# Kernel optimization log

Measured on AMD Instinct MI355X. Metric: run time of the kernel, lower is better.

## Reference

```python
import jax, jax.numpy as jnp
import numpy as np
from jax import lax

N_IN = 512      # n_input == n_output of decoder
N_H = 2048      # n_hidden
N_L = 2         # n_layers (encoder/decoder GRU stacks written out explicitly)
SEQ = 2048      # sequence length
SPARSITY = 0.1  # sparsity_level -> k_sparse = int(N_H * SPARSITY)


def setup_inputs() -> dict:
    key = jax.random.key(0)
    ks = jax.random.split(key, 14)
    s = 0.02
    f32 = jnp.float32
    return {
        "sequence": jax.random.normal(ks[0], (SEQ, N_IN), f32),
        # encoder GRU (pytorch layout: W_ih [3H, in], W_hh [3H, H], gate order r,z,n)
        "enc_Wih0": jax.random.normal(ks[1], (3 * N_H, N_IN), f32) * s,
        "enc_Wih1": jax.random.normal(ks[2], (3 * N_H, N_H), f32) * s,
        "enc_Whh": jax.random.normal(ks[3], (N_L, 3 * N_H, N_H), f32) * s,
        "enc_bih": jax.random.normal(ks[4], (N_L, 3 * N_H), f32) * s,
        "enc_bhh": jax.random.normal(ks[5], (N_L, 3 * N_H), f32) * s,
        # decoder GRU (input dim = N_IN)
        "dec_Wih0": jax.random.normal(ks[6], (3 * N_H, N_IN), f32) * s,
        "dec_Wih1": jax.random.normal(ks[7], (3 * N_H, N_H), f32) * s,
        "dec_Whh": jax.random.normal(ks[8], (N_L, 3 * N_H, N_H), f32) * s,
        "dec_bih": jax.random.normal(ks[9], (N_L, 3 * N_H), f32) * s,
        "dec_bhh": jax.random.normal(ks[10], (N_L, 3 * N_H), f32) * s,
        # decoder output Linear: n_hidden -> n_output
        "dec_Wout": jax.random.normal(ks[11], (N_IN, N_H), f32) * s,
        "dec_bout": jax.random.normal(ks[12], (N_IN,), f32) * s,
    }


def _gru_cell(x, h, Wih, Whh, bih, bhh):
    # x: [in], h: [H]; PyTorch GRU equations, gate order (r, z, n)
    gi = Wih @ x + bih
    gh = Whh @ h + bhh
    ir, iz, inn = jnp.split(gi, 3)
    hr, hz, hn = jnp.split(gh, 3)
    r = jax.nn.sigmoid(ir + hr)
    z = jax.nn.sigmoid(iz + hz)
    n = jnp.tanh(inn + r * hn)
    return (1.0 - z) * n + z * h


def reference(sequence, enc_Wih0, enc_Wih1, enc_Whh, enc_bih, enc_bhh,
              dec_Wih0, dec_Wih1, dec_Whh, dec_bih, dec_bhh,
              dec_Wout, dec_bout):
    seq_len = sequence.shape[0]

    # ---- encoder: 2-layer GRU over the sequence, batch=1 (batch dim dropped) ----
    def enc_step(h, x):
        h0 = _gru_cell(x, h[0], enc_Wih0, enc_Whh[0], enc_bih[0], enc_bhh[0])
        h1 = _gru_cell(h0, h[1], enc_Wih1, enc_Whh[1], enc_bih[1], enc_bhh[1])
        return jnp.stack([h0, h1]), None

    h0_init = jnp.zeros((N_L, N_H), sequence.dtype)
    enc_hidden, _ = lax.scan(enc_step, h0_init, sequence)

    # ---- top-k sparsity on innermost (last) layer of the hidden state ----
    k_sparse = int(N_H * SPARSITY)
    h_last = enc_hidden[N_L - 1]
    _, top_idx = lax.top_k(h_last, k_sparse)
    mask = jnp.zeros((N_H,), h_last.dtype).at[top_idx].set(1.0)
    enc_hidden = enc_hidden.at[N_L - 1].set(h_last * mask)

    # ---- decoder: seq_len-1 single-step GRU+Linear, targets are sequence reversed ----
    targets = jnp.flip(sequence[: seq_len - 1], axis=0)  # sequence[seq_len-2-i]

    def dec_step(carry, target):
        x, h = carry
        h0 = _gru_cell(x, h[0], dec_Wih0, dec_Whh[0], dec_bih[0], dec_bhh[0])
        h1 = _gru_cell(h0, h[1], dec_Wih1, dec_Whh[1], dec_bih[1], dec_bhh[1])
        out = dec_Wout @ h1 + dec_bout
        step_loss = jnp.mean((out - target) ** 2)
        return (out, jnp.stack([h0, h1])), (out, step_loss)

    init = (sequence[seq_len - 1], enc_hidden)
    _, (reconstructed, step_losses) = lax.scan(dec_step, init, targets)
    loss = jnp.sum(step_losses) / seq_len
    return reconstructed, loss
```

## Files before the change

kernel.cpp:

```cpp
#include <hip/hip_runtime.h>
#include <hip/hip_fp16.h>
#include <hip/hip_cooperative_groups.h>

namespace cg = cooperative_groups;

#define H      2048
#define NIN    512
#define TH     (3 * H)
#define SEQLEN 2048
#define KSP    204
#define NBLK   256
#define NTHR   512

typedef unsigned int uint32;

constexpr long O_EA = 0;
constexpr long O_EB = O_EA + 1572864;
constexpr long O_EC = O_EB + 6291456;
constexpr long O_ED = O_EC + 6291456;
constexpr long O_DA = O_ED + 6291456;
constexpr long O_DB = O_DA + 1572864;
constexpr long O_DC = O_DB + 6291456;
constexpr long O_DD = O_DC + 6291456;
constexpr long O_WO = O_DD + 6291456;
constexpr long U_TOTAL = O_WO + 524288;
constexpr size_t WS_STATE_BYTES = 65536;

struct Params {
    const float* seq;
    const float* eWih0; const float* eWih1; const float* eWhh;
    const float* ebih;  const float* ebhh;
    const float* dWih0; const float* dWih1; const float* dWhh;
    const float* dbih;  const float* dbhh;
    const float* dWout; const float* dbout;
    float* out;
    float* ws;
};

__device__ __forceinline__ float wave_reduce_f(float v) {
#pragma unroll
    for (int m = 32; m >= 1; m >>= 1) v += __shfl_xor(v, m, 64);
    return v;
}

__device__ __forceinline__ float sigmoidf_(float v) { return 1.f / (1.f + expf(-v)); }

__device__ __forceinline__ float2 h2f(uint32 u) {
    __half2 h = *reinterpret_cast<__half2*>(&u);
    return __half22float2(h);
}

__global__ void pack_kernel(const float* __restrict__ src, uint32* __restrict__ dst,
                            int total, int xdim, int nrows)
{
    int KK = xdim / 256;
    for (int i = blockIdx.x * blockDim.x + threadIdx.x; i < total;
         i += gridDim.x * blockDim.x) {
        int l = i & 63;
        int rest = i >> 6;
        int p2 = rest & 1; rest >>= 1;
        int kk = rest % KK; rest /= KK;
        int r  = rest % nrows; rest /= nrows;
        int j  = rest;
        int c0 = 256 * kk + 4 * l + 2 * p2;
        const float* row = src + ((size_t)r * H + j) * xdim;
        unsigned short b0 = __half_as_ushort(__float2half_rn(row[c0]));
        unsigned short b1 = __half_as_ushort(__float2half_rn(row[c0 + 1]));
        dst[i] = ((uint32)b1 << 16) | b0;
    }
}

template <int NU>
__device__ __forceinline__ void load_seg3(uint32 (&dst)[3][NU], const uint32* seg,
                                          int j, int lane)
{
#pragma unroll
    for (int r = 0; r < 3; ++r)
#pragma unroll
        for (int u = 0; u < NU; ++u)
            dst[r][u] = seg[((size_t)(j * 3 + r) * NU + u) * 64 + lane];
}

__device__ __forceinline__ void load_seg1(uint32 (&dst)[16], const uint32* seg,
                                          int j, int lane)
{
#pragma unroll
    for (int u = 0; u < 16; ++u)
        dst[u] = seg[((size_t)j * 16 + u) * 64 + lane];
}

template <int NU>
__device__ __forceinline__ void dot3h(const uint32 (&w)[3][NU],
                                      const float* __restrict__ vec, int lane,
                                      float acc[3])
{
#pragma unroll
    for (int kk = 0; kk < NU / 2; ++kk) {
        float4 v = ((const float4*)vec)[kk * 64 + lane];
#pragma unroll
        for (int r = 0; r < 3; ++r) {
            float2 lo = h2f(w[r][2 * kk]);
            float2 hi = h2f(w[r][2 * kk + 1]);
            acc[r] = fmaf(lo.x, v.x, acc[r]);
            acc[r] = fmaf(lo.y, v.y, acc[r]);
            acc[r] = fmaf(hi.x, v.z, acc[r]);
            acc[r] = fmaf(hi.y, v.w, acc[r]);
        }
    }
}

template <int NUX>
__device__ __forceinline__ float gru_cell_reg(int j, int lane,
    const uint32 (&wi)[3][NUX], const uint32 (&wh)[3][16],
    const float* __restrict__ x, const float* __restrict__ h,
    float bir, float biz, float bin, float bhr, float bhz, float bhn)
{
    float ai[3] = {0.f, 0.f, 0.f}, ah[3] = {0.f, 0.f, 0.f};
    dot3h<NUX>(wi, x, lane, ai);
    dot3h<16>(wh, h, lane, ah);
    float hj  = h[j];
    float sr  = wave_reduce_f(ai[0] + ah[0]);
    float sz  = wave_reduce_f(ai[1] + ah[1]);
    float sn  = wave_reduce_f(ai[2]);
    float shn = wave_reduce_f(ah[2]);
    float r = sigmoidf_(sr + bir + bhr);
    float z = sigmoidf_(sz + biz + bhz);
    float n = tanhf(sn + bin + r * (shn + bhn));
    return (1.f - z) * n + z * hj;
}

__global__ void __launch_bounds__(NTHR, 2)
seqae_reg_kernel(Params p)
{
    cg::grid_group grid = cg::this_grid();
    const int lane = threadIdx.x & 63;
    const int j    = blockIdx.x * (NTHR / 64) + (threadIdx.x >> 6);

    float* loss = p.ws;
    float* h0b[2] = { p.ws + 64, p.ws + 64 + H };
    float* h1b[2] = { p.ws + 64 + 2 * H, p.ws + 64 + 3 * H };
    const uint32* U = (const uint32*)((const char*)p.ws + WS_STATE_BYTES);

    {
        int gtid = blockIdx.x * NTHR + threadIdx.x;
        if (gtid == 0) *loss = 0.f;
        for (int i = gtid; i < H; i += NBLK * NTHR) { h0b[0][i] = 0.f; h1b[0][i] = 0.f; }
    }
    grid.sync();

    uint32 wa[3][4], wb[3][16], wc[3][16], wd[3][16];
    load_seg3<4>(wa, U + O_EA, j, lane);
    load_seg3<16>(wb, U + O_EB, j, lane);
    load_seg3<16>(wc, U + O_EC, j, lane);
    load_seg3<16>(wd, U + O_ED, j, lane);

    float eb[12];
    {
        const float* bi0 = p.ebih;      const float* bi1 = p.ebih + TH;
        const float* bh0 = p.ebhh;      const float* bh1 = p.ebhh + TH;
        eb[0] = bi0[j]; eb[1] = bi0[H + j]; eb[2] = bi0[2 * H + j];
        eb[3] = bh0[j]; eb[4] = bh0[H + j]; eb[5] = bh0[2 * H + j];
        eb[6] = bi1[j]; eb[7] = bi1[H + j]; eb[8] = bi1[2 * H + j];
        eb[9] = bh1[j]; eb[10] = bh1[H + j]; eb[11] = bh1[2 * H + j];
    }

    int c0 = 0, c1 = 0;

    for (int ph = 0; ph <= SEQLEN; ++ph) {
        const float* h0old = h0b[c0];
        float h0v = 0.f, h1v = 0.f;
        if (ph < SEQLEN)
            h0v = gru_cell_reg<4>(j, lane, wa, wb, p.seq + (size_t)ph * NIN, h0old,
                                  eb[0], eb[1], eb[2], eb[3], eb[4], eb[5]);
        if (ph >= 1)
            h1v = gru_cell_reg<16>(j, lane, wc, wd, h0old, h1b[c1],
                                   eb[6], eb[7], eb[8], eb[9], eb[10], eb[11]);
        if (lane == 0) {
            if (ph < SEQLEN) h0b[c0 ^ 1][j] = h0v;
            if (ph >= 1)     h1b[c1 ^ 1][j] = h1v;
        }
        grid.sync();
        if (ph < SEQLEN) c0 ^= 1;
        if (ph >= 1)     c1 ^= 1;
    }

    {
        const float* hs = h1b[c1];
        float vj = hs[j];
        int cnt = 0;
        for (int i = lane; i < H; i += 64) {
            float vi = hs[i];
            cnt += (vi > vj) || (vi == vj && i < j);
        }
#pragma unroll
        for (int m = 32; m >= 1; m >>= 1) cnt += __shfl_xor(cnt, m, 64);
        if (lane == 0) h1b[c1 ^ 1][j] = (cnt < KSP) ? vj : 0.f;
    }
    grid.sync();
    c1 ^= 1;

    load_seg3<4>(wa, U + O_DA, j, lane);
    load_seg3<16>(wb, U + O_DB, j, lane);
    load_seg3<16>(wc, U + O_DC, j, lane);
    load_seg3<16>(wd, U + O_DD, j, lane);
    uint32 wo[16];
    load_seg1(wo, U + O_WO, j & (NIN - 1), lane);

    float db[12], boutj;
    {
        const float* bi0 = p.dbih;      const float* bi1 = p.dbih + TH;
        const float* bh0 = p.dbhh;      const float* bh1 = p.dbhh + TH;
        db[0] = bi0[j]; db[1] = bi0[H + j]; db[2] = bi0[2 * H + j];
        db[3] = bh0[j]; db[4] = bh0[H + j]; db[5] = bh0[2 * H + j];
        db[6] = bi1[j]; db[7] = bi1[H + j]; db[8] = bi1[2 * H + j];
        db[9] = bh1[j]; db[10] = bh1[H + j]; db[11] = bh1[2 * H + j];
        boutj = p.dbout[j & (NIN - 1)];
    }

    float lsum = 0.f;
    for (int t = 0; t < SEQLEN - 1; ++t) {
        const float* x = (t == 0) ? (p.seq + (size_t)(SEQLEN - 1) * NIN)
                                  : (p.out + (size_t)(t - 1) * NIN);
        float h0v = gru_cell_reg<4>(j, lane, wa, wb, x, h0b[c0],
                                    db[0], db[1], db[2], db[3], db[4], db[5]);
        if (lane == 0) h0b[c0 ^ 1][j] = h0v;
        grid.sync(); c0 ^= 1;

        float h1v = gru_cell_reg<16>(j, lane, wc, wd, h0b[c0], h1b[c1],
                                     db[6], db[7], db[8], db[9], db[10], db[11]);
        if (lane == 0) h1b[c1 ^ 1][j] = h1v;
        grid.sync(); c1 ^= 1;

        if (j < NIN) {
            const float* h1n = h1b[c1];
            float a = 0.f;
#pragma unroll
            for (int kk = 0; kk < 8; ++kk) {
                float4 v = ((const float4*)h1n)[kk * 64 + lane];
                float2 lo = h2f(wo[2 * kk]);
                float2 hi = h2f(wo[2 * kk + 1]);
                a = fmaf(lo.x, v.x, a); a = fmaf(lo.y, v.y, a);
                a = fmaf(hi.x, v.z, a); a = fmaf(hi.y, v.w, a);
            }
            a = wave_reduce_f(a);
            float o = a + boutj;
            if (lane == 0) p.out[(size_t)t * NIN + j] = o;
            float tg = p.seq[(size_t)(SEQLEN - 2 - t) * NIN + j];
            float d = o - tg;
            lsum = fmaf(d, d, lsum);
        }
        grid.sync();
    }

    if (j < NIN && lane == 0) atomicAdd(loss, lsum);
    grid.sync();
    if (blockIdx.x == 0 && threadIdx.x == 0)
        p.out[(size_t)(SEQLEN - 1) * NIN] = (*loss) * (1.f / ((float)NIN * (float)SEQLEN));
}

template <int XDIM>
__device__ __forceinline__ void gru_phase_fb(int j, int lane,
    const float* __restrict__ Wih, const float* __restrict__ Whh,
    const float* __restrict__ bih, const float* __restrict__ bhh,
    const float* __restrict__ x,
    const float* __restrict__ hcur, float* __restrict__ hnxt)
{
    const float4* wir = (const float4*)(Wih + (size_t)j * XDIM);
    const float4* wiz = (const float4*)(Wih + (size_t)(H + j) * XDIM);
    const float4* win = (const float4*)(Wih + (size_t)(2 * H + j) * XDIM);
    const float4* whr = (const float4*)(Whh + (size_t)j * H);
    const float4* whz = (const float4*)(Whh + (size_t)(H + j) * H);
    const float4* whn = (const float4*)(Whh + (size_t)(2 * H + j) * H);
    const float4* x4  = (const float4*)x;
    const float4* h4  = (const float4*)hcur;

    float air = 0.f, aiz = 0.f, ain = 0.f;
#pragma unroll
    for (int k = 0; k < XDIM / 256; ++k) {
        int i = lane + 64 * k;
        float4 xv = x4[i];
        float4 a = wir[i], b = wiz[i], c = win[i];
        air = fmaf(a.x, xv.x, air); air = fmaf(a.y, xv.y, air);
        air = fmaf(a.z, xv.z, air); air = fmaf(a.w, xv.w, air);
        aiz = fmaf(b.x, xv.x, aiz); aiz = fmaf(b.y, xv.y, aiz);
        aiz = fmaf(b.z, xv.z, aiz); aiz = fmaf(b.w, xv.w, aiz);
        ain = fmaf(c.x, xv.x, ain); ain = fmaf(c.y, xv.y, ain);
        ain = fmaf(c.z, xv.z, ain); ain = fmaf(c.w, xv.w, ain);
    }
    float ahr = 0.f, ahz = 0.f, ahn = 0.f;
#pragma unroll
    for (int k = 0; k < H / 256; ++k) {
        int i = lane + 64 * k;
        float4 hv = h4[i];
        float4 a = whr[i], b = whz[i], c = whn[i];
        ahr = fmaf(a.x, hv.x, ahr); ahr = fmaf(a.y, hv.y, ahr);
        ahr = fmaf(a.z, hv.z, ahr); ahr = fmaf(a.w, hv.w, ahr);
        ahz = fmaf(b.x, hv.x, ahz); ahz = fmaf(b.y, hv.y, ahz);
        ahz = fmaf(b.z, hv.z, ahz); ahz = fmaf(b.w, hv.w, ahz);
        ahn = fmaf(c.x, hv.x, ahn); ahn = fmaf(c.y, hv.y, ahn);
        ahn = fmaf(c.z, hv.z, ahn); ahn = fmaf(c.w, hv.w, ahn);
    }
    float sr   = wave_reduce_f(air + ahr);
    float sz   = wave_reduce_f(aiz + ahz);
    float sin_ = wave_reduce_f(ain);
    float shn  = wave_reduce_f(ahn);

    if (lane == 0) {
        float r = sigmoidf_(sr + bih[j] + bhh[j]);
        float z = sigmoidf_(sz + bih[H + j] + bhh[H + j]);
        float n = tanhf(sin_ + bih[2 * H + j] + r * (shn + bhh[2 * H + j]));
        hnxt[j] = (1.f - z) * n + z * hcur[j];
    }
}

__global__ void __launch_bounds__(NTHR)
seqae_fallback_kernel(Params p)
{
    cg::grid_group grid = cg::this_grid();
    const int lane = threadIdx.x & 63;
    const int wid  = blockIdx.x * (NTHR / 64) + (threadIdx.x >> 6);

    float* loss = p.ws;
    float* h0a  = p.ws + 64;
    float* h0b  = h0a + H;
    float* h1a  = h0b + H;
    float* h1b  = h1a + H;

    {
        int gtid = blockIdx.x * NTHR + threadIdx.x;
        if (gtid == 0) *loss = 0.f;
        for (int i = gtid; i < H; i += NBLK * NTHR) { h0a[i] = 0.f; h1a[i] = 0.f; }
    }
    grid.sync();

    const float* ebih0 = p.ebih;        const float* ebih1 = p.ebih + TH;
    const float* ebhh0 = p.ebhh;        const float* ebhh1 = p.ebhh + TH;
    const float* eWhh0 = p.eWhh;        const float* eWhh1 = p.eWhh + (size_t)TH * H;

    float* h0c = h0a; float* h0n = h0b;
    float* h1c = h1a; float* h1n = h1b;

    for (int t = 0; t < SEQLEN; ++t) {
        const float* x = p.seq + (size_t)t * NIN;
        gru_phase_fb<NIN>(wid, lane, p.eWih0, eWhh0, ebih0, ebhh0, x, h0c, h0n);
        grid.sync();
        gru_phase_fb<H>(wid, lane, p.eWih1, eWhh1, ebih1, ebhh1, h0n, h1c, h1n);
        grid.sync();
        float* tmp;
        tmp = h0c; h0c = h0n; h0n = tmp;
        tmp = h1c; h1c = h1n; h1n = tmp;
    }

    {
        int j = wid;
        float vj = h1c[j];
        int cnt = 0;
        for (int i = lane; i < H; i += 64) {
            float vi = h1c[i];
            cnt += (vi > vj) || (vi == vj && i < j);
        }
#pragma unroll
        for (int m = 32; m >= 1; m >>= 1) cnt += __shfl_xor(cnt, m, 64);
        if (lane == 0) h1n[j] = (cnt < KSP) ? vj : 0.f;
    }
    grid.sync();
    { float* tmp = h1c; h1c = h1n; h1n = tmp; }

    const float* dbih0 = p.dbih;        const float* dbih1 = p.dbih + TH;
    const float* dbhh0 = p.dbhh;        const float* dbhh1 = p.dbhh + TH;
    const float* dWhh0 = p.dWhh;        const float* dWhh1 = p.dWhh + (size_t)TH * H;

    float lsum = 0.f;
    for (int t = 0; t < SEQLEN - 1; ++t) {
        const float* x = (t == 0) ? (p.seq + (size_t)(SEQLEN - 1) * NIN)
                                  : (p.out + (size_t)(t - 1) * NIN);
        gru_phase_fb<NIN>(wid, lane, p.dWih0, dWhh0, dbih0, dbhh0, x, h0c, h0n);
        grid.sync();
        gru_phase_fb<H>(wid, lane, p.dWih1, dWhh1, dbih1, dbhh1, h0n, h1c, h1n);
        grid.sync();
        if (wid < NIN) {
            int j = wid;
            const float4* wo = (const float4*)(p.dWout + (size_t)j * H);
            const float4* h4 = (const float4*)h1n;
            float a = 0.f;
#pragma unroll
            for (int k = 0; k < H / 256; ++k) {
                int i = lane + 64 * k;
                float4 w = wo[i]; float4 hv = h4[i];
                a = fmaf(w.x, hv.x, a); a = fmaf(w.y, hv.y, a);
                a = fmaf(w.z, hv.z, a); a = fmaf(w.w, hv.w, a);
            }
            a = wave_reduce_f(a);
            if (lane == 0) {
                float o = a + p.dbout[j];
                p.out[(size_t)t * NIN + j] = o;
                float tg = p.seq[(size_t)(SEQLEN - 2 - t) * NIN + j];
                float d = o - tg;
                lsum = fmaf(d, d, lsum);
            }
        }
        grid.sync();
        float* tmp;
        tmp = h0c; h0c = h0n; h0n = tmp;
        tmp = h1c; h1c = h1n; h1n = tmp;
    }

    if (wid < NIN && lane == 0) atomicAdd(loss, lsum);
    grid.sync();
    if (blockIdx.x == 0 && threadIdx.x == 0) {
        p.out[(size_t)(SEQLEN - 1) * NIN] = (*loss) * (1.f / ((float)NIN * (float)SEQLEN));
    }
}

extern "C" void kernel_launch(void* const* d_in, const int* in_sizes, int n_in,
                              void* d_out, int out_size, void* d_ws, size_t ws_size,
                              hipStream_t stream)
{
    Params p;
    p.seq   = (const float*)d_in[0];
    p.eWih0 = (const float*)d_in[1];
    p.eWih1 = (const float*)d_in[2];
    p.eWhh  = (const float*)d_in[3];
    p.ebih  = (const float*)d_in[4];
    p.ebhh  = (const float*)d_in[5];
    p.dWih0 = (const float*)d_in[6];
    p.dWih1 = (const float*)d_in[7];
    p.dWhh  = (const float*)d_in[8];
    p.dbih  = (const float*)d_in[9];
    p.dbhh  = (const float*)d_in[10];
    p.dWout = (const float*)d_in[11];
    p.dbout = (const float*)d_in[12];
    p.out = (float*)d_out;
    p.ws  = (float*)d_ws;

    size_t need = WS_STATE_BYTES + (size_t)U_TOTAL * 4;
    if (ws_size >= need) {
        uint32* U = (uint32*)((char*)d_ws + WS_STATE_BYTES);
        const int PB = 256, PG = 1024;
        pack_kernel<<<PG, PB, 0, stream>>>(p.eWih0, U + O_EA, 1572864, NIN, 3);
        pack_kernel<<<PG, PB, 0, stream>>>(p.eWhh,  U + O_EB, 6291456, H, 3);
        pack_kernel<<<PG, PB, 0, stream>>>(p.eWih1, U + O_EC, 6291456, H, 3);
        pack_kernel<<<PG, PB, 0, stream>>>(p.eWhh + (size_t)TH * H, U + O_ED, 6291456, H, 3);
        pack_kernel<<<PG, PB, 0, stream>>>(p.dWih0, U + O_DA, 1572864, NIN, 3);
        pack_kernel<<<PG, PB, 0, stream>>>(p.dWhh,  U + O_DB, 6291456, H, 3);
        pack_kernel<<<PG, PB, 0, stream>>>(p.dWih1, U + O_DC, 6291456, H, 3);
        pack_kernel<<<PG, PB, 0, stream>>>(p.dWhh + (size_t)TH * H, U + O_DD, 6291456, H, 3);
        pack_kernel<<<PG, PB, 0, stream>>>(p.dWout, U + O_WO, 524288, H, 1);

        void* args[] = { &p };
        (void)hipLaunchCooperativeKernel((void*)seqae_reg_kernel, dim3(NBLK), dim3(NTHR),
                                         args, 0, stream);
    } else {
        void* args[] = { &p };
        (void)hipLaunchCooperativeKernel((void*)seqae_fallback_kernel, dim3(NBLK), dim3(NTHR),
                                         args, 0, stream);
    }
}
```

Before: 370.6 ms.

## Split GRU layers across two wave groups per block with 1024 threads

The persistent cooperative kernel now launches 1024 threads per block. The first eight waves handle layer 0 and the last eight handle layer 1 for the same hidden units, so each wave keeps only one layer's fp16 weights in registers (96 uint32) instead of both layers' weights. This halves per-wave register pressure and serial dot-product work per encoder step, and doubles the number of waves doing useful work in parallel. In the decoder, half the waves sit idle in each phase, and __launch_bounds__(1024,4) may force register spills.

Result: slower. 393.7 ms (+6.2%).

```diff
diff --git a/kernel.cpp b/kernel.cpp
--- a/kernel.cpp
+++ b/kernel.cpp
@@ -10,7 +10,8 @@
 #define SEQLEN 2048
 #define KSP    204
 #define NBLK   256
-#define NTHR   512
+#define NTHR_S 1024
+#define NTHR_F 512
 
 typedef unsigned int uint32;
 
@@ -26,28 +27,18 @@
 constexpr long U_TOTAL = O_WO + 524288;
 constexpr size_t WS_STATE_BYTES = 65536;
 
-struct Params {
-    const float* seq;
-    const float* eWih0; const float* eWih1; const float* eWhh;
-    const float* ebih;  const float* ebhh;
-    const float* dWih0; const float* dWih1; const float* dWhh;
-    const float* dbih;  const float* dbhh;
-    const float* dWout; const float* dbout;
-    float* out;
-    float* ws;
-};
-
 __device__ __forceinline__ float wave_reduce_f(float v) {
 #pragma unroll
     for (int m = 32; m >= 1; m >>= 1) v += __shfl_xor(v, m, 64);
     return v;
 }
-
 __device__ __forceinline__ float sigmoidf_(float v) { return 1.f / (1.f + expf(-v)); }
-
 __device__ __forceinline__ float2 h2f(uint32 u) {
     __half2 h = *reinterpret_cast<__half2*>(&u);
     return __half22float2(h);
+}
+__device__ __forceinline__ float rfl(float x) {
+    return __uint_as_float(__builtin_amdgcn_readfirstlane(__float_as_uint(x)));
 }
 
 __global__ void pack_kernel(const float* __restrict__ src, uint32* __restrict__ dst,
@@ -70,114 +61,118 @@
     }
 }
 
-template <int NU>
-__device__ __forceinline__ void load_seg3(uint32 (&dst)[3][NU], const uint32* seg,
-                                          int j, int lane)
+template <int BASE, int NU>
+__device__ __forceinline__ void loadw(uint32 (&w)[96], const uint32* __restrict__ seg,
+                                      int j, int lane)
 {
 #pragma unroll
     for (int r = 0; r < 3; ++r)
 #pragma unroll
         for (int u = 0; u < NU; ++u)
-            dst[r][u] = seg[((size_t)(j * 3 + r) * NU + u) * 64 + lane];
-}
-
-__device__ __forceinline__ void load_seg1(uint32 (&dst)[16], const uint32* seg,
-                                          int j, int lane)
+            w[BASE + r * NU + u] = seg[((size_t)(j * 3 + r) * NU + u) * 64 + lane];
+}
+__device__ __forceinline__ void loadwo(uint32 (&w)[96], const uint32* __restrict__ seg,
+                                       int j, int lane)
 {
 #pragma unroll
     for (int u = 0; u < 16; ++u)
-        dst[u] = seg[((size_t)j * 16 + u) * 64 + lane];
-}
-
-template <int NU>
-__device__ __forceinline__ void dot3h(const uint32 (&w)[3][NU],
-                                      const float* __restrict__ vec, int lane,
-                                      float acc[3])
+        w[60 + u] = seg[((size_t)j * 16 + u) * 64 + lane];
+}
+
+template <int BASE, int NU>
+__device__ __forceinline__ void dot3(const uint32 (&w)[96],
+                                     const float* __restrict__ vec, int lane,
+                                     float acc[3])
 {
 #pragma unroll
     for (int kk = 0; kk < NU / 2; ++kk) {
         float4 v = ((const float4*)vec)[kk * 64 + lane];
 #pragma unroll
         for (int r = 0; r < 3; ++r) {
-            float2 lo = h2f(w[r][2 * kk]);
-            float2 hi = h2f(w[r][2 * kk + 1]);
-            acc[r] = fmaf(lo.x, v.x, acc[r]);
-            acc[r] = fmaf(lo.y, v.y, acc[r]);
-            acc[r] = fmaf(hi.x, v.z, acc[r]);
-            acc[r] = fmaf(hi.y, v.w, acc[r]);
-        }
-    }
-}
-
-template <int NUX>
-__device__ __forceinline__ float gru_cell_reg(int j, int lane,
-    const uint32 (&wi)[3][NUX], const uint32 (&wh)[3][16],
+            float2 lo = h2f(w[BASE + r * NU + 2 * kk]);
+            float2 hi = h2f(w[BASE + r * NU + 2 * kk + 1]);
+            acc[r] = fmaf(lo.x, v.x, acc[r]); acc[r] = fmaf(lo.y, v.y, acc[r]);
+            acc[r] = fmaf(hi.x, v.z, acc[r]); acc[r] = fmaf(hi.y, v.w, acc[r]);
+        }
+    }
+}
+
+template <int BI, int NI>
+__device__ __forceinline__ float cellu(const uint32 (&w)[96], int j, int lane,
     const float* __restrict__ x, const float* __restrict__ h,
     float bir, float biz, float bin, float bhr, float bhz, float bhn)
 {
-    float ai[3] = {0.f, 0.f, 0.f}, ah[3] = {0.f, 0.f, 0.f};
-    dot3h<NUX>(wi, x, lane, ai);
-    dot3h<16>(wh, h, lane, ah);
+    float gi[3] = {0.f, 0.f, 0.f};
+    dot3<BI, NI>(w, x, lane, gi);
+    float gh[3] = {0.f, 0.f, 0.f};
+    dot3<BI + 3 * NI, 16>(w, h, lane, gh);
     float hj  = h[j];
-    float sr  = wave_reduce_f(ai[0] + ah[0]);
-    float sz  = wave_reduce_f(ai[1] + ah[1]);
-    float sn  = wave_reduce_f(ai[2]);
-    float shn = wave_reduce_f(ah[2]);
+    float sr  = wave_reduce_f(gi[0] + gh[0]);
+    float sz  = wave_reduce_f(gi[1] + gh[1]);
+    float sn  = wave_reduce_f(gi[2]);
+    float shn = wave_reduce_f(gh[2]);
     float r = sigmoidf_(sr + bir + bhr);
     float z = sigmoidf_(sz + biz + bhz);
     float n = tanhf(sn + bin + r * (shn + bhn));
     return (1.f - z) * n + z * hj;
 }
 
-__global__ void __launch_bounds__(NTHR, 2)
-seqae_reg_kernel(Params p)
+__global__ void __launch_bounds__(NTHR_S, 4)
+seqae_split_kernel(const float* __restrict__ seq,
+                   const uint32* __restrict__ U,
+                   const float* __restrict__ ebih, const float* __restrict__ ebhh,
+                   const float* __restrict__ dbih, const float* __restrict__ dbhh,
+                   const float* __restrict__ dbout,
+                   float* __restrict__ out,
+                   float* __restrict__ wsf)
 {
     cg::grid_group grid = cg::this_grid();
     const int lane = threadIdx.x & 63;
-    const int j    = blockIdx.x * (NTHR / 64) + (threadIdx.x >> 6);
-
-    float* loss = p.ws;
-    float* h0b[2] = { p.ws + 64, p.ws + 64 + H };
-    float* h1b[2] = { p.ws + 64 + 2 * H, p.ws + 64 + 3 * H };
-    const uint32* U = (const uint32*)((const char*)p.ws + WS_STATE_BYTES);
+    const int wv   = threadIdx.x >> 6;
+    const bool g1  = (wv >= 8);
+    const int j    = blockIdx.x * 8 + (wv & 7);
+
+    float* loss = wsf;
+    float* h0b[2] = { wsf + 64, wsf + 64 + H };
+    float* h1b[2] = { wsf + 64 + 2 * H, wsf + 64 + 3 * H };
 
     {
-        int gtid = blockIdx.x * NTHR + threadIdx.x;
+        int gtid = blockIdx.x * NTHR_S + threadIdx.x;
         if (gtid == 0) *loss = 0.f;
-        for (int i = gtid; i < H; i += NBLK * NTHR) { h0b[0][i] = 0.f; h1b[0][i] = 0.f; }
+        for (int i = gtid; i < H; i += NBLK * NTHR_S) { h0b[0][i] = 0.f; h1b[0][i] = 0.f; }
     }
     grid.sync();
 
-    uint32 wa[3][4], wb[3][16], wc[3][16], wd[3][16];
-    load_seg3<4>(wa, U + O_EA, j, lane);
-    load_seg3<16>(wb, U + O_EB, j, lane);
-    load_seg3<16>(wc, U + O_EC, j, lane);
-    load_seg3<16>(wd, U + O_ED, j, lane);
-
-    float eb[12];
-    {
-        const float* bi0 = p.ebih;      const float* bi1 = p.ebih + TH;
-        const float* bh0 = p.ebhh;      const float* bh1 = p.ebhh + TH;
-        eb[0] = bi0[j]; eb[1] = bi0[H + j]; eb[2] = bi0[2 * H + j];
-        eb[3] = bh0[j]; eb[4] = bh0[H + j]; eb[5] = bh0[2 * H + j];
-        eb[6] = bi1[j]; eb[7] = bi1[H + j]; eb[8] = bi1[2 * H + j];
-        eb[9] = bh1[j]; eb[10] = bh1[H + j]; eb[11] = bh1[2 * H + j];
+    uint32 wreg[96];
+    float b0, b1, b2, b3, b4, b5;
+    if (!g1) {
+        loadw<0, 4>(wreg, U + O_EA, j, lane);
+        loadw<12, 16>(wreg, U + O_EB, j, lane);
+        b0 = rfl(ebih[j]); b1 = rfl(ebih[H + j]); b2 = rfl(ebih[2 * H + j]);
+        b3 = rfl(ebhh[j]); b4 = rfl(ebhh[H + j]); b5 = rfl(ebhh[2 * H + j]);
+    } else {
+        loadw<0, 16>(wreg, U + O_EC, j, lane);
+        loadw<48, 16>(wreg, U + O_ED, j, lane);
+        const float* bi = ebih + TH; const float* bh = ebhh + TH;
+        b0 = rfl(bi[j]); b1 = rfl(bi[H + j]); b2 = rfl(bi[2 * H + j]);
+        b3 = rfl(bh[j]); b4 = rfl(bh[H + j]); b5 = rfl(bh[2 * H + j]);
     }
 
     int c0 = 0, c1 = 0;
 
     for (int ph = 0; ph <= SEQLEN; ++ph) {
-        const float* h0old = h0b[c0];
-        float h0v = 0.f, h1v = 0.f;
-        if (ph < SEQLEN)
-            h0v = gru_cell_reg<4>(j, lane, wa, wb, p.seq + (size_t)ph * NIN, h0old,
-                                  eb[0], eb[1], eb[2], eb[3], eb[4], eb[5]);
-        if (ph >= 1)
-            h1v = gru_cell_reg<16>(j, lane, wc, wd, h0old, h1b[c1],
-                                   eb[6], eb[7], eb[8], eb[9], eb[10], eb[11]);
-        if (lane == 0) {
-            if (ph < SEQLEN) h0b[c0 ^ 1][j] = h0v;
-            if (ph >= 1)     h1b[c1 ^ 1][j] = h1v;
+        if (!g1) {
+            if (ph < SEQLEN) {
+                float v = cellu<0, 4>(wreg, j, lane, seq + (size_t)ph * NIN, h0b[c0],
+                                      b0, b1, b2, b3, b4, b5);
+                if (lane == 0) h0b[c0 ^ 1][j] = v;
+            }
+        } else {
+            if (ph >= 1) {
+                float v = cellu<0, 16>(wreg, j, lane, h0b[c0], h1b[c1],
+                                       b0, b1, b2, b3, b4, b5);
+                if (lane == 0) h1b[c1 ^ 1][j] = v;
+            }
         }
         grid.sync();
         if (ph < SEQLEN) c0 ^= 1;
@@ -186,77 +181,89 @@
 
     {
         const float* hs = h1b[c1];
-        float vj = hs[j];
-        int cnt = 0;
-        for (int i = lane; i < H; i += 64) {
-            float vi = hs[i];
-            cnt += (vi > vj) || (vi == vj && i < j);
-        }
-#pragma unroll
-        for (int m = 32; m >= 1; m >>= 1) cnt += __shfl_xor(cnt, m, 64);
-        if (lane == 0) h1b[c1 ^ 1][j] = (cnt < KSP) ? vj : 0.f;
-    }
-    grid.sync();
-    c1 ^= 1;
-
-    load_seg3<4>(wa, U + O_DA, j, lane);
-    load_seg3<16>(wb, U + O_DB, j, lane);
-    load_seg3<16>(wc, U + O_DC, j, lane);
-    load_seg3<16>(wd, U + O_DD, j, lane);
-    uint32 wo[16];
-    load_seg1(wo, U + O_WO, j & (NIN - 1), lane);
-
-    float db[12], boutj;
-    {
-        const float* bi0 = p.dbih;      const float* bi1 = p.dbih + TH;
-        const float* bh0 = p.dbhh;      const float* bh1 = p.dbhh + TH;
-        db[0] = bi0[j]; db[1] = bi0[H + j]; db[2] = bi0[2 * H + j];
-        db[3] = bh0[j]; db[4] = bh0[H + j]; db[5] = bh0[2 * H + j];
-        db[6] = bi1[j]; db[7] = bi1[H + j]; db[8] = bi1[2 * H + j];
-        db[9] = bh1[j]; db[10] = bh1[H + j]; db[11] = bh1[2 * H + j];
-        boutj = p.dbout[j & (NIN - 1)];
+        if (!g1) {
+            float vj = hs[j];
+            int cnt = 0;
+            for (int i = lane; i < H; i += 64) {
+                float vi = hs[i];
+                cnt += (vi > vj) || (vi == vj && i < j);
+            }
+#pragma unroll
+            for (int m = 32; m >= 1; m >>= 1) cnt += __shfl_xor(cnt, m, 64);
+            if (lane == 0) h1b[c1 ^ 1][j] = (cnt < KSP) ? vj : 0.f;
+        }
+        grid.sync();
+        c1 ^= 1;
+    }
+
+    float boutj = 0.f;
+    if (!g1) {
+        loadw<0, 4>(wreg, U + O_DA, j, lane);
+        loadw<12, 16>(wreg, U + O_DB, j, lane);
+        if (j < NIN) { loadwo(wreg, U + O_WO, j, lane); boutj = rfl(dbout[j]); }
+        b0 = rfl(dbih[j]); b1 = rfl(dbih[H + j]); b2 = rfl(dbih[2 * H + j]);
+        b3 = rfl(dbhh[j]); b4 = rfl(dbhh[H + j]); b5 = rfl(dbhh[2 * H + j]);
+    } else {
+        loadw<0, 16>(wreg, U + O_DC, j, lane);
+        loadw<48, 16>(wreg, U + O_DD, j, lane);
+        const float* bi = dbih + TH; const float* bh = dbhh + TH;
+        b0 = rfl(bi[j]); b1 = rfl(bi[H + j]); b2 = rfl(bi[2 * H + j]);
+        b3 = rfl(bh[j]); b4 = rfl(bh[H + j]); b5 = rfl(bh[2 * H + j]);
     }
 
     float lsum = 0.f;
     for (int t = 0; t < SEQLEN - 1; ++t) {
-        const float* x = (t == 0) ? (p.seq + (size_t)(SEQLEN - 1) * NIN)
-                                  : (p.out + (size_t)(t - 1) * NIN);
-        float h0v = gru_cell_reg<4>(j, lane, wa, wb, x, h0b[c0],
-                                    db[0], db[1], db[2], db[3], db[4], db[5]);
-        if (lane == 0) h0b[c0 ^ 1][j] = h0v;
+        if (!g1) {
+            const float* x = (t == 0) ? (seq + (size_t)(SEQLEN - 1) * NIN)
+                                      : (out + (size_t)(t - 1) * NIN);
+            float v = cellu<0, 4>(wreg, j, lane, x, h0b[c0], b0, b1, b2, b3, b4, b5);
+            if (lane == 0) h0b[c0 ^ 1][j] = v;
+        }
         grid.sync(); c0 ^= 1;
 
-        float h1v = gru_cell_reg<16>(j, lane, wc, wd, h0b[c0], h1b[c1],
-                                     db[6], db[7], db[8], db[9], db[10], db[11]);
-        if (lane == 0) h1b[c1 ^ 1][j] = h1v;
+        if (g1) {
+            float v = cellu<0, 16>(wreg, j, lane, h0b[c0], h1b[c1], b0, b1, b2, b3, b4, b5);
+            if (lane == 0) h1b[c1 ^ 1][j] = v;
+        }
         grid.sync(); c1 ^= 1;
 
-        if (j < NIN) {
+        if (!g1 && j < NIN) {
             const float* h1n = h1b[c1];
             float a = 0.f;
 #pragma unroll
             for (int kk = 0; kk < 8; ++kk) {
                 float4 v = ((const float4*)h1n)[kk * 64 + lane];
-                float2 lo = h2f(wo[2 * kk]);
-                float2 hi = h2f(wo[2 * kk + 1]);
+                float2 lo = h2f(wreg[60 + 2 * kk]);
+                float2 hi = h2f(wreg[60 + 2 * kk + 1]);
                 a = fmaf(lo.x, v.x, a); a = fmaf(lo.y, v.y, a);
                 a = fmaf(hi.x, v.z, a); a = fmaf(hi.y, v.w, a);
             }
             a = wave_reduce_f(a);
             float o = a + boutj;
-            if (lane == 0) p.out[(size_t)t * NIN + j] = o;
-            float tg = p.seq[(size_t)(SEQLEN - 2 - t) * NIN + j];
+            if (lane == 0) out[(size_t)t * NIN + j] = o;
+            float tg = seq[(size_t)(SEQLEN - 2 - t) * NIN + j];
             float d = o - tg;
             lsum = fmaf(d, d, lsum);
         }
         grid.sync();
     }
 
-    if (j < NIN && lane == 0) atomicAdd(loss, lsum);
+    if (!g1 && j < NIN && lane == 0) atomicAdd(loss, lsum);
     grid.sync();
     if (blockIdx.x == 0 && threadIdx.x == 0)
-        p.out[(size_t)(SEQLEN - 1) * NIN] = (*loss) * (1.f / ((float)NIN * (float)SEQLEN));
-}
+        out[(size_t)(SEQLEN - 1) * NIN] = (*loss) * (1.f / ((float)NIN * (float)SEQLEN));
+}
+
+struct Params {
+    const float* seq;
+    const float* eWih0; const float* eWih1; const float* eWhh;
+    const float* ebih;  const float* ebhh;
+    const float* dWih0; const float* dWih1; const float* dWhh;
+    const float* dbih;  const float* dbhh;
+    const float* dWout; const float* dbout;
+    float* out;
+    float* ws;
+};
 
 template <int XDIM>
 __device__ __forceinline__ void gru_phase_fb(int j, int lane,
@@ -313,12 +320,12 @@
     }
 }
 
-__global__ void __launch_bounds__(NTHR)
+__global__ void __launch_bounds__(NTHR_F)
 seqae_fallback_kernel(Params p)
 {
     cg::grid_group grid = cg::this_grid();
     const int lane = threadIdx.x & 63;
-    const int wid  = blockIdx.x * (NTHR / 64) + (threadIdx.x >> 6);
+    const int wid  = blockIdx.x * (NTHR_F / 64) + (threadIdx.x >> 6);
 
     float* loss = p.ws;
     float* h0a  = p.ws + 64;
@@ -327,9 +334,9 @@
     float* h1b  = h1a + H;
 
     {
-        int gtid = blockIdx.x * NTHR + threadIdx.x;
+        int gtid = blockIdx.x * NTHR_F + threadIdx.x;
         if (gtid == 0) *loss = 0.f;
-        for (int i = gtid; i < H; i += NBLK * NTHR) { h0a[i] = 0.f; h1a[i] = 0.f; }
+        for (int i = gtid; i < H; i += NBLK * NTHR_F) { h0a[i] = 0.f; h1a[i] = 0.f; }
     }
     grid.sync();
 
@@ -352,16 +359,16 @@
     }
 
     {
-        int j = wid;
-        float vj = h1c[j];
+        int jj = wid;
+        float vj = h1c[jj];
         int cnt = 0;
         for (int i = lane; i < H; i += 64) {
             float vi = h1c[i];
-            cnt += (vi > vj) || (vi == vj && i < j);
+            cnt += (vi > vj) || (vi == vj && i < jj);
         }
 #pragma unroll
         for (int m = 32; m >= 1; m >>= 1) cnt += __shfl_xor(cnt, m, 64);
-        if (lane == 0) h1n[j] = (cnt < KSP) ? vj : 0.f;
+        if (lane == 0) h1n[jj] = (cnt < KSP) ? vj : 0.f;
     }
     grid.sync();
     { float* tmp = h1c; h1c = h1n; h1n = tmp; }
@@ -379,8 +386,8 @@
         gru_phase_fb<H>(wid, lane, p.dWih1, dWhh1, dbih1, dbhh1, h0n, h1c, h1n);
         grid.sync();
         if (wid < NIN) {
-            int j = wid;
-            const float4* wo = (const float4*)(p.dWout + (size_t)j * H);
+            int jj = wid;
+            const float4* wo = (const float4*)(p.dWout + (size_t)jj * H);
             const float4* h4 = (const float4*)h1n;
             float a = 0.f;
 #pragma unroll
@@ -392,9 +399,9 @@
             }
             a = wave_reduce_f(a);
             if (lane == 0) {
-                float o = a + p.dbout[j];
-                p.out[(size_t)t * NIN + j] = o;
-                float tg = p.seq[(size_t)(SEQLEN - 2 - t) * NIN + j];
+                float o = a + p.dbout[jj];
+                p.out[(size_t)t * NIN + jj] = o;
+                float tg = p.seq[(size_t)(SEQLEN - 2 - t) * NIN + jj];
                 float d = o - tg;
                 lsum = fmaf(d, d, lsum);
             }
@@ -416,43 +423,50 @@
                               void* d_out, int out_size, void* d_ws, size_t ws_size,
                               hipStream_t stream)
 {
-    Params p;
-    p.seq   = (const float*)d_in[0];
-    p.eWih0 = (const float*)d_in[1];
-    p.eWih1 = (const float*)d_in[2];
-    p.eWhh  = (const float*)d_in[3];
-    p.ebih  = (const float*)d_in[4];
-    p.ebhh  = (const float*)d_in[5];
-    p.dWih0 = (const float*)d_in[6];
-    p.dWih1 = (const float*)d_in[7];
-    p.dWhh  = (const float*)d_in[8];
-    p.dbih  = (const float*)d_in[9];
-    p.dbhh  = (const float*)d_in[10];
-    p.dWout = (const float*)d_in[11];
-    p.dbout = (const float*)d_in[12];
-    p.out = (float*)d_out;
-    p.ws  = (float*)d_ws;
+    const float* seq   = (const float*)d_in[0];
+    const float* eWih0 = (const float*)d_in[1];
+    const float* eWih1 = (const float*)d_in[2];
+    const float* eWhh  = (const float*)d_in[3];
+    const float* ebih  = (const float*)d_in[4];
+    const float* ebhh  = (const float*)d_in[5];
+    const float* dWih0 = (const float*)d_in[6];
+    const float* dWih1 = (const float*)d_in[7];
+    const float* dWhh  = (const float*)d_in[8];
+    const float* dbih  = (const float*)d_in[9];
+    const float* dbhh  = (const float*)d_in[10];
+    const float* dWout = (const float*)d_in[11];
+    const float* dbout = (const float*)d_in[12];
+    float* out = (float*)d_out;
+    float* wsf = (float*)d_ws;
 
     size_t need = WS_STATE_BYTES + (size_t)U_TOTAL * 4;
     if (ws_size >= need) {
         uint32* U = (uint32*)((char*)d_ws + WS_STATE_BYTES);
         const int PB = 256, PG = 1024;
-        pack_kernel<<<PG, PB, 0, stream>>>(p.eWih0, U + O_EA, 1572864, NIN, 3);
-        pack_kernel<<<PG, PB, 0, stream>>>(p.eWhh,  U + O_EB, 6291456, H, 3);
-        pack_kernel<<<PG, PB, 0, stream>>>(p.eWih1, U + O_EC, 6291456, H, 3);
-        pack_kernel<<<PG, PB, 0, stream>>>(p.eWhh + (size_t)TH * H, U + O_ED, 6291456, H, 3);
-        pack_kernel<<<PG, PB, 0, stream>>>(p.dWih0, U + O_DA, 1572864, NIN, 3);
-        pack_kernel<<<PG, PB, 0, stream>>>(p.dWhh,  U + O_DB, 6291456, H, 3);
-        pack_kernel<<<PG, PB, 0, stream>>>(p.dWih1, U + O_DC, 6291456, H, 3);
-        pack_kernel<<<PG, PB, 0, stream>>>(p.dWhh + (size_t)TH * H, U + O_DD, 6291456, H, 3);
-        pack_kernel<<<PG, PB, 0, stream>>>(p.dWout, U + O_WO, 524288, H, 1);
-
-        void* args[] = { &p };
-        (void)hipLaunchCooperativeKernel((void*)seqae_reg_kernel, dim3(NBLK), dim3(NTHR),
+        pack_kernel<<<PG, PB, 0, stream>>>(eWih0, U + O_EA, 1572864, NIN, 3);
+        pack_kernel<<<PG, PB, 0, stream>>>(eWhh,  U + O_EB, 6291456, H, 3);
+        pack_kernel<<<PG, PB, 0, stream>>>(eWih1, U + O_EC, 6291456, H, 3);
+        pack_kernel<<<PG, PB, 0, stream>>>(eWhh + (size_t)TH * H, U + O_ED, 6291456, H, 3);
+        pack_kernel<<<PG, PB, 0, stream>>>(dWih0, U + O_DA, 1572864, NIN, 3);
+        pack_kernel<<<PG, PB, 0, stream>>>(dWhh,  U + O_DB, 6291456, H, 3);
+        pack_kernel<<<PG, PB, 0, stream>>>(dWih1, U + O_DC, 6291456, H, 3);
+        pack_kernel<<<PG, PB, 0, stream>>>(dWhh + (size_t)TH * H, U + O_DD, 6291456, H, 3);
+        pack_kernel<<<PG, PB, 0, stream>>>(dWout, U + O_WO, 524288, H, 1);
+
+        const uint32* Uc = U;
+        void* args[] = { &seq, &Uc, &ebih, &ebhh, &dbih, &dbhh, &dbout, &out, &wsf };
+        (void)hipLaunchCooperativeKernel((void*)seqae_split_kernel, dim3(NBLK), dim3(NTHR_S),
                                          args, 0, stream);
     } else {
+        Params p;
+        p.seq = seq; p.eWih0 = eWih0; p.eWih1 = eWih1; p.eWhh = eWhh;
+        p.ebih = ebih; p.ebhh = ebhh;
+        p.dWih0 = dWih0; p.dWih1 = dWih1; p.dWhh = dWhh;
+        p.dbih = dbih; p.dbhh = dbhh;
+        p.dWout = dWout; p.dbout = dbout;
+        p.out = out; p.ws = wsf;
         void* args[] = { &p };
-        (void)hipLaunchCooperativeKernel((void*)seqae_fallback_kernel, dim3(NBLK), dim3(NTHR),
+        (void)hipLaunchCooperativeKernel((void*)seqae_fallback_kernel, dim3(NBLK), dim3(NTHR_F),
                                          args, 0, stream);
     }
 }
```
